# Optimization experiments

Measured on AMD Instinct MI355X. Metric: run time of the kernel, lower is better.

The kernel has to match this reference:

```python
import jax, jax.numpy as jnp
import numpy as np

H = 256  # rnn_size


def setup_inputs() -> dict:
    key = jax.random.key(0)
    ks = jax.random.split(key, 6)
    B, T, F, D = 64, 512, 64, 64
    s_in = 1.0 / np.sqrt(F)
    s_rec = 1.0 / np.sqrt(H)
    return {
        "x": jax.random.normal(ks[0], (B, T, F), jnp.float32),
        "kernel": jax.random.normal(ks[1], (F, 3 * H), jnp.float32) * s_in,
        "recurrent_kernel": jax.random.normal(ks[2], (H, 3 * H), jnp.float32) * s_rec,
        "bias": jax.random.normal(ks[3], (3 * H,), jnp.float32) * 0.01,
        "dense_w": jax.random.normal(ks[4], (H, D), jnp.float32) * s_rec,
        "dense_b": jax.random.normal(ks[5], (D,), jnp.float32) * 0.01,
    }


def _gru_scan(x, kernel, recurrent_kernel, bias):
    B, T, _ = x.shape
    # Pre-project all timesteps: [B, T, 3H]
    xproj = jnp.einsum("btf,fg->btg", x, kernel) + bias
    xproj_t = jnp.transpose(xproj, (1, 0, 2))  # [T, B, 3H]

    def step(h, xt):
        # Keras GRU, reset_after=False: r gates the recurrent matmul of the candidate
        rec = h @ recurrent_kernel  # [B, 3H]
        xz, xr, xh = xt[:, :H], xt[:, H:2 * H], xt[:, 2 * H:]
        rz, rr, rh = rec[:, :H], rec[:, H:2 * H], rec[:, 2 * H:]
        z = jax.nn.sigmoid(xz + rz)
        r = jax.nn.sigmoid(xr + rr)
        hh = jnp.tanh(xh + r * rh)
        h_new = z * h + (1.0 - z) * hh
        return h_new, h_new

    h0 = jnp.zeros((B, H), x.dtype)
    h_last, outs = jax.lax.scan(step, h0, xproj_t)
    return jnp.transpose(outs, (1, 0, 2)), h_last  # [B,T,H], [B,H]


def reference(x, kernel, recurrent_kernel, bias, dense_w, dense_b):
    outputs, h_last = _gru_scan(x, kernel, recurrent_kernel, bias)
    state = jnp.tanh(h_last @ dense_w + dense_b)  # [B, dense_size]
    return outputs, state
```

## Files before the change

kernel.cpp:

```cpp
#include <hip/hip_runtime.h>


typedef _Float16 half2_t __attribute__((ext_vector_type(2)));
typedef _Float16 f16x4_t __attribute__((ext_vector_type(4)));

#define LOG2E 1.4426950408889634f

__device__ __forceinline__ float fast_sigmoid(float x) {
  float e = __builtin_amdgcn_exp2f(-x * LOG2E);
  return __builtin_amdgcn_rcpf(1.0f + e);
}
__device__ __forceinline__ float fast_tanh(float x) {
  float e = __builtin_amdgcn_exp2f(x * (2.0f * LOG2E));
  return 1.0f - 2.0f * __builtin_amdgcn_rcpf(1.0f + e);
}

__global__ __launch_bounds__(256, 4) void xproj_gemm(
    const float* __restrict__ x, const float* __restrict__ kmat,
    const float* __restrict__ bias, _Float16* __restrict__ xp) {
  __shared__ half2_t As2[32][132];
  __shared__ half2_t Bs2[32][132];
  const int tid = threadIdx.x;
  const int rb = blockIdx.x * 128;
  const int cb = blockIdx.y * 128;

  {
    const int k4 = (tid & 15) * 4;
    const int r0 = tid >> 4;
#pragma unroll
    for (int p = 0; p < 8; ++p) {
      int r = r0 + p * 16;
      float4 v = *(const float4*)(x + (size_t)(rb + r) * 64 + k4);
      half2_t lo, hi;
      lo[0] = (_Float16)v.x; lo[1] = (_Float16)v.y;
      hi[0] = (_Float16)v.z; hi[1] = (_Float16)v.w;
      As2[k4 / 2][r] = lo;
      As2[k4 / 2 + 1][r] = hi;
    }
  }
  {
    const int c4 = (tid & 31) * 4;
    const int kp0 = tid >> 5;
#pragma unroll
    for (int p = 0; p < 4; ++p) {
      int kp = kp0 + p * 8;
      float4 va = *(const float4*)(kmat + (size_t)(2 * kp) * 768 + cb + c4);
      float4 vb = *(const float4*)(kmat + (size_t)(2 * kp + 1) * 768 + cb + c4);
      half2_t o0, o1, o2, o3;
      o0[0] = (_Float16)va.x; o0[1] = (_Float16)vb.x;
      o1[0] = (_Float16)va.y; o1[1] = (_Float16)vb.y;
      o2[0] = (_Float16)va.z; o2[1] = (_Float16)vb.z;
      o3[0] = (_Float16)va.w; o3[1] = (_Float16)vb.w;
      Bs2[kp][c4 + 0] = o0;
      Bs2[kp][c4 + 1] = o1;
      Bs2[kp][c4 + 2] = o2;
      Bs2[kp][c4 + 3] = o3;
    }
  }
  __syncthreads();

  const int tx = tid & 15, ty = tid >> 4;
  const int r0 = ty * 8;
  const int c0 = tx * 4;
  float acc[8][8];
  {
    float4 b0 = *(const float4*)(bias + cb + c0);
    float4 b1 = *(const float4*)(bias + cb + 64 + c0);
    float bz[8] = {b0.x, b0.y, b0.z, b0.w, b1.x, b1.y, b1.z, b1.w};
#pragma unroll
    for (int i = 0; i < 8; ++i)
#pragma unroll
      for (int j = 0; j < 8; ++j) acc[i][j] = bz[j];
  }

#pragma unroll 2
  for (int kp = 0; kp < 32; ++kp) {
    half2_t a2[8], b2[8];
    *(int4*)(&a2[0]) = *(const int4*)(&As2[kp][r0]);
    *(int4*)(&a2[4]) = *(const int4*)(&As2[kp][r0 + 4]);
    *(int2*)(&b2[0]) = *(const int2*)(&Bs2[kp][c0]);
    *(int2*)(&b2[2]) = *(const int2*)(&Bs2[kp][c0 + 2]);
    *(int2*)(&b2[4]) = *(const int2*)(&Bs2[kp][64 + c0]);
    *(int2*)(&b2[6]) = *(const int2*)(&Bs2[kp][64 + c0 + 2]);
#pragma unroll
    for (int i = 0; i < 8; ++i)
#pragma unroll
      for (int j = 0; j < 8; ++j)
        acc[i][j] = __builtin_amdgcn_fdot2(a2[i], b2[j], acc[i][j], false);
  }

#pragma unroll
  for (int i = 0; i < 8; ++i) {
    f16x4_t o0, o1;
#pragma unroll
    for (int j = 0; j < 4; ++j) {
      o0[j] = (_Float16)acc[i][j];
      o1[j] = (_Float16)acc[i][4 + j];
    }
    _Float16* dst = xp + (size_t)(rb + r0 + i) * 768 + cb;
    *(f16x4_t*)(dst + c0) = o0;
    *(f16x4_t*)(dst + 64 + c0) = o1;
  }
}

__global__ __launch_bounds__(1024, 4) void gru_scan(
    const _Float16* __restrict__ xp, const float* __restrict__ wr,
    const float* __restrict__ dw, const float* __restrict__ db,
    float* __restrict__ out, float* __restrict__ state) {
  __shared__ float2 part2[768 * 3];
  __shared__ float hbuf[256];
  __shared__ alignas(16) _Float16 hhalf[256];

  const int tid = threadIdx.x;
  const int b = blockIdx.x;
  const int c = tid >> 8;
  const int col = tid & 255;

  half2_t w2[3][32];
#pragma unroll
  for (int q = 0; q < 3; ++q) {
    const float* wp = wr + (size_t)(c * 64) * 768 + col + q * 256;
#pragma unroll
    for (int j = 0; j < 32; ++j) {
      float wa = wp[(size_t)(2 * j) * 768];
      float wb = wp[(size_t)(2 * j + 1) * 768];
      half2_t p;
      p[0] = (_Float16)wa;
      p[1] = (_Float16)wb;
      w2[q][j] = p;
    }
  }
#pragma unroll
  for (int q = 0; q < 3; ++q)
#pragma unroll
    for (int j = 0; j < 32; ++j) asm volatile("" : "+v"(w2[q][j]));

  if (tid < 256) hhalf[tid] = (_Float16)0.0f;
  __syncthreads();

  const _Float16* xpb = xp + (size_t)b * 512 * 768;
  float* outb = out + (size_t)b * 512 * 256;
  const int4* hp2 = (const int4*)hhalf + c * 8;
  float* pw = (float*)part2;
  float hprev = 0.0f;

#pragma unroll 1
  for (int t = 0; t < 512; ++t) {
    _Float16 x0 = (_Float16)0.0f, x1 = (_Float16)0.0f, x2 = (_Float16)0.0f;
    if (tid < 256) {
      if (t) outb[(size_t)(t - 1) * 256 + tid] = hprev;
      const _Float16* xr = xpb + (size_t)t * 768 + tid;
      x0 = xr[0];
      x1 = xr[256];
      x2 = xr[512];
    }

    float a0 = 0.0f, a1 = 0.0f, a2 = 0.0f;
#pragma unroll
    for (int g = 0; g < 8; ++g) {
      int4 hv = hp2[g];
      half2_t p0 = __builtin_bit_cast(half2_t, hv.x);
      half2_t p1 = __builtin_bit_cast(half2_t, hv.y);
      half2_t p2 = __builtin_bit_cast(half2_t, hv.z);
      half2_t p3 = __builtin_bit_cast(half2_t, hv.w);
      a0 = __builtin_amdgcn_fdot2(p0, w2[0][g * 4 + 0], a0, false);
      a0 = __builtin_amdgcn_fdot2(p1, w2[0][g * 4 + 1], a0, false);
      a0 = __builtin_amdgcn_fdot2(p2, w2[0][g * 4 + 2], a0, false);
      a0 = __builtin_amdgcn_fdot2(p3, w2[0][g * 4 + 3], a0, false);
      a1 = __builtin_amdgcn_fdot2(p0, w2[1][g * 4 + 0], a1, false);
      a1 = __builtin_amdgcn_fdot2(p1, w2[1][g * 4 + 1], a1, false);
      a1 = __builtin_amdgcn_fdot2(p2, w2[1][g * 4 + 2], a1, false);
      a1 = __builtin_amdgcn_fdot2(p3, w2[1][g * 4 + 3], a1, false);
      a2 = __builtin_amdgcn_fdot2(p0, w2[2][g * 4 + 0], a2, false);
      a2 = __builtin_amdgcn_fdot2(p1, w2[2][g * 4 + 1], a2, false);
      a2 = __builtin_amdgcn_fdot2(p2, w2[2][g * 4 + 2], a2, false);
      a2 = __builtin_amdgcn_fdot2(p3, w2[2][g * 4 + 3], a2, false);
    }
    pw[col * 6 + c] = a0;
    pw[1536 + col * 6 + c] = a1;
    pw[3072 + col * 6 + c] = a2;
    __syncthreads();

    if (tid < 256) {
      const int i = tid;
      float2 z0 = part2[i * 3 + 0];
      float2 z1 = part2[i * 3 + 1];
      float2 r0 = part2[768 + i * 3 + 0];
      float2 r1 = part2[768 + i * 3 + 1];
      float2 h0 = part2[1536 + i * 3 + 0];
      float2 h1 = part2[1536 + i * 3 + 1];
      float rz = (z0.x + z0.y) + (z1.x + z1.y);
      float rr = (r0.x + r0.y) + (r1.x + r1.y);
      float rh = (h0.x + h0.y) + (h1.x + h1.y);
      float z = fast_sigmoid((float)x0 + rz);
      float r = fast_sigmoid((float)x1 + rr);
      float hh = fast_tanh((float)x2 + r * rh);
      float hnew = z * hprev + (1.0f - z) * hh;
      hprev = hnew;
      hhalf[i] = (_Float16)hnew;
    }
    __syncthreads();
  }

  if (tid < 256) {
    outb[(size_t)511 * 256 + tid] = hprev;
    hbuf[tid] = hprev;
  }
  __syncthreads();

  if (tid < 64) {
    float acc = db[tid];
#pragma unroll 8
    for (int k = 0; k < 256; ++k) acc = fmaf(hbuf[k], dw[k * 64 + tid], acc);
    state[(size_t)b * 64 + tid] = fast_tanh(acc);
  }
}

extern "C" void kernel_launch(void* const* d_in, const int* in_sizes, int n_in,
                              void* d_out, int out_size, void* d_ws,
                              size_t ws_size, hipStream_t stream) {
  const float* x = (const float*)d_in[0];
  const float* kmat = (const float*)d_in[1];
  const float* wr = (const float*)d_in[2];
  const float* bias = (const float*)d_in[3];
  const float* dw = (const float*)d_in[4];
  const float* db = (const float*)d_in[5];

  float* out = (float*)d_out;
  float* state = out + (size_t)64 * 512 * 256;
  _Float16* xp = (_Float16*)d_ws;

  dim3 gg(32768 / 128, 768 / 128);
  xproj_gemm<<<gg, 256, 0, stream>>>(x, kmat, bias, xp);
  gru_scan<<<64, 1024, 0, stream>>>(xp, wr, dw, db, out, state);
}
```

Measured before the change: 660.9 us.

## Process four batch rows per block in GRU scan, reusing register weights

Each scan block now handles four batch sequences, reusing the per-thread fp16 recurrent weights held in registers across all four. Each thread computes partial matvecs for all four batches and then runs the gate update for its own batch element, so all 1024 threads do elementwise work. The grid shrinks from 64 to 16 blocks, which quadruples the serial per-step dot-product work and enlarges shared memory. The empty asm statements that kept the weights pinned in registers are also removed.

New measurement: 2.055 ms. 211% more time.

```diff
diff --git a/kernel.cpp b/kernel.cpp
--- a/kernel.cpp
+++ b/kernel.cpp
@@ -107,19 +107,19 @@
     const _Float16* __restrict__ xp, const float* __restrict__ wr,
     const float* __restrict__ dw, const float* __restrict__ db,
     float* __restrict__ out, float* __restrict__ state) {
-  __shared__ float2 part2[768 * 3];
-  __shared__ float hbuf[256];
-  __shared__ alignas(16) _Float16 hhalf[256];
+  __shared__ float pw[4 * 768 * 6];
+  __shared__ alignas(16) _Float16 hhalf[4][256];
+  __shared__ float hbuf[4][256];
 
   const int tid = threadIdx.x;
-  const int b = blockIdx.x;
-  const int c = tid >> 8;
+  const int bg = blockIdx.x;
+  const int kc = tid >> 8;
   const int col = tid & 255;
 
   half2_t w2[3][32];
 #pragma unroll
   for (int q = 0; q < 3; ++q) {
-    const float* wp = wr + (size_t)(c * 64) * 768 + col + q * 256;
+    const float* wp = wr + (size_t)(kc * 64) * 768 + col + q * 256;
 #pragma unroll
     for (int j = 0; j < 32; ++j) {
       float wa = wp[(size_t)(2 * j) * 768];
@@ -130,65 +130,64 @@
       w2[q][j] = p;
     }
   }
-#pragma unroll
-  for (int q = 0; q < 3; ++q)
-#pragma unroll
-    for (int j = 0; j < 32; ++j) asm volatile("" : "+v"(w2[q][j]));
-
-  if (tid < 256) hhalf[tid] = (_Float16)0.0f;
+
+  hhalf[kc][col] = (_Float16)0.0f;
   __syncthreads();
 
-  const _Float16* xpb = xp + (size_t)b * 512 * 768;
-  float* outb = out + (size_t)b * 512 * 256;
-  const int4* hp2 = (const int4*)hhalf + c * 8;
-  float* pw = (float*)part2;
+  const _Float16* xpb = xp + (size_t)(bg * 4 + kc) * 512 * 768;
+  float* outb = out + (size_t)(bg * 4 + kc) * 512 * 256;
   float hprev = 0.0f;
 
 #pragma unroll 1
   for (int t = 0; t < 512; ++t) {
-    _Float16 x0 = (_Float16)0.0f, x1 = (_Float16)0.0f, x2 = (_Float16)0.0f;
-    if (tid < 256) {
-      if (t) outb[(size_t)(t - 1) * 256 + tid] = hprev;
-      const _Float16* xr = xpb + (size_t)t * 768 + tid;
-      x0 = xr[0];
-      x1 = xr[256];
-      x2 = xr[512];
-    }
-
-    float a0 = 0.0f, a1 = 0.0f, a2 = 0.0f;
-#pragma unroll
-    for (int g = 0; g < 8; ++g) {
-      int4 hv = hp2[g];
-      half2_t p0 = __builtin_bit_cast(half2_t, hv.x);
-      half2_t p1 = __builtin_bit_cast(half2_t, hv.y);
-      half2_t p2 = __builtin_bit_cast(half2_t, hv.z);
-      half2_t p3 = __builtin_bit_cast(half2_t, hv.w);
-      a0 = __builtin_amdgcn_fdot2(p0, w2[0][g * 4 + 0], a0, false);
-      a0 = __builtin_amdgcn_fdot2(p1, w2[0][g * 4 + 1], a0, false);
-      a0 = __builtin_amdgcn_fdot2(p2, w2[0][g * 4 + 2], a0, false);
-      a0 = __builtin_amdgcn_fdot2(p3, w2[0][g * 4 + 3], a0, false);
-      a1 = __builtin_amdgcn_fdot2(p0, w2[1][g * 4 + 0], a1, false);
-      a1 = __builtin_amdgcn_fdot2(p1, w2[1][g * 4 + 1], a1, false);
-      a1 = __builtin_amdgcn_fdot2(p2, w2[1][g * 4 + 2], a1, false);
-      a1 = __builtin_amdgcn_fdot2(p3, w2[1][g * 4 + 3], a1, false);
-      a2 = __builtin_amdgcn_fdot2(p0, w2[2][g * 4 + 0], a2, false);
-      a2 = __builtin_amdgcn_fdot2(p1, w2[2][g * 4 + 1], a2, false);
-      a2 = __builtin_amdgcn_fdot2(p2, w2[2][g * 4 + 2], a2, false);
-      a2 = __builtin_amdgcn_fdot2(p3, w2[2][g * 4 + 3], a2, false);
-    }
-    pw[col * 6 + c] = a0;
-    pw[1536 + col * 6 + c] = a1;
-    pw[3072 + col * 6 + c] = a2;
+    _Float16 x0, x1, x2;
+    {
+      if (t) outb[(size_t)(t - 1) * 256 + col] = hprev;
+      const _Float16* xq = xpb + (size_t)t * 768 + col;
+      x0 = xq[0];
+      x1 = xq[256];
+      x2 = xq[512];
+    }
+
+#pragma unroll
+    for (int b = 0; b < 4; ++b) {
+      const int4* hp = (const int4*)&hhalf[b][0] + kc * 8;
+      float a0 = 0.0f, a1 = 0.0f, a2 = 0.0f;
+#pragma unroll
+      for (int g = 0; g < 8; ++g) {
+        int4 hv = hp[g];
+        half2_t p0 = __builtin_bit_cast(half2_t, hv.x);
+        half2_t p1 = __builtin_bit_cast(half2_t, hv.y);
+        half2_t p2 = __builtin_bit_cast(half2_t, hv.z);
+        half2_t p3 = __builtin_bit_cast(half2_t, hv.w);
+        a0 = __builtin_amdgcn_fdot2(p0, w2[0][g * 4 + 0], a0, false);
+        a0 = __builtin_amdgcn_fdot2(p1, w2[0][g * 4 + 1], a0, false);
+        a0 = __builtin_amdgcn_fdot2(p2, w2[0][g * 4 + 2], a0, false);
+        a0 = __builtin_amdgcn_fdot2(p3, w2[0][g * 4 + 3], a0, false);
+        a1 = __builtin_amdgcn_fdot2(p0, w2[1][g * 4 + 0], a1, false);
+        a1 = __builtin_amdgcn_fdot2(p1, w2[1][g * 4 + 1], a1, false);
+        a1 = __builtin_amdgcn_fdot2(p2, w2[1][g * 4 + 2], a1, false);
+        a1 = __builtin_amdgcn_fdot2(p3, w2[1][g * 4 + 3], a1, false);
+        a2 = __builtin_amdgcn_fdot2(p0, w2[2][g * 4 + 0], a2, false);
+        a2 = __builtin_amdgcn_fdot2(p1, w2[2][g * 4 + 1], a2, false);
+        a2 = __builtin_amdgcn_fdot2(p2, w2[2][g * 4 + 2], a2, false);
+        a2 = __builtin_amdgcn_fdot2(p3, w2[2][g * 4 + 3], a2, false);
+      }
+      float* pb = pw + b * 4608;
+      pb[(size_t)col * 6 + kc] = a0;
+      pb[(size_t)(256 + col) * 6 + kc] = a1;
+      pb[(size_t)(512 + col) * 6 + kc] = a2;
+    }
     __syncthreads();
 
-    if (tid < 256) {
-      const int i = tid;
-      float2 z0 = part2[i * 3 + 0];
-      float2 z1 = part2[i * 3 + 1];
-      float2 r0 = part2[768 + i * 3 + 0];
-      float2 r1 = part2[768 + i * 3 + 1];
-      float2 h0 = part2[1536 + i * 3 + 0];
-      float2 h1 = part2[1536 + i * 3 + 1];
+    {
+      const float2* pb = (const float2*)(pw + kc * 4608);
+      float2 z0 = pb[col * 3 + 0];
+      float2 z1 = pb[col * 3 + 1];
+      float2 r0 = pb[(256 + col) * 3 + 0];
+      float2 r1 = pb[(256 + col) * 3 + 1];
+      float2 h0 = pb[(512 + col) * 3 + 0];
+      float2 h1 = pb[(512 + col) * 3 + 1];
       float rz = (z0.x + z0.y) + (z1.x + z1.y);
       float rr = (r0.x + r0.y) + (r1.x + r1.y);
       float rh = (h0.x + h0.y) + (h1.x + h1.y);
@@ -197,22 +196,23 @@
       float hh = fast_tanh((float)x2 + r * rh);
       float hnew = z * hprev + (1.0f - z) * hh;
       hprev = hnew;
-      hhalf[i] = (_Float16)hnew;
+      hhalf[kc][col] = (_Float16)hnew;
     }
     __syncthreads();
   }
 
+  outb[(size_t)511 * 256 + col] = hprev;
+  hbuf[kc][col] = hprev;
+  __syncthreads();
+
   if (tid < 256) {
-    outb[(size_t)511 * 256 + tid] = hprev;
-    hbuf[tid] = hprev;
-  }
-  __syncthreads();
-
-  if (tid < 64) {
-    float acc = db[tid];
+    const int bt = tid >> 6;
+    const int d = tid & 63;
+    float acc = db[d];
 #pragma unroll 8
-    for (int k = 0; k < 256; ++k) acc = fmaf(hbuf[k], dw[k * 64 + tid], acc);
-    state[(size_t)b * 64 + tid] = fast_tanh(acc);
+    for (int k = 0; k < 256; ++k)
+      acc = fmaf(hbuf[bt][k], dw[k * 64 + d], acc);
+    state[(size_t)(bg * 4 + bt) * 64 + d] = fast_tanh(acc);
   }
 }
 
@@ -232,5 +232,5 @@
 
   dim3 gg(32768 / 128, 768 / 128);
   xproj_gemm<<<gg, 256, 0, stream>>>(x, kmat, bias, xp);
-  gru_scan<<<64, 1024, 0, stream>>>(xp, wr, dw, db, out, state);
-}
+  gru_scan<<<16, 1024, 0, stream>>>(xp, wr, dw, db, out, state);
+}
```

## Rewrite input projection GEMM with MFMA 16x16x32 f16 instructions

Applied to the files above, without the earlier changes.

Replaces the LDS-tiled fdot2 input projection GEMM with a register-only MFMA version. Each wave loads A and B fragments straight from global memory, converts them to fp16 and runs mfma_f32_16x16x32_f16, then adds the bias and stores fp16. This drops the shared-memory staging and the __syncthreads, and the output stores now become strided 2-byte writes. The serial gru_scan kernel most likely dominates total time, so the overall effect is limited.

New measurement: 654.5 us. About the same (-1.0%).

```diff
diff --git a/kernel.cpp b/kernel.cpp
--- a/kernel.cpp
+++ b/kernel.cpp
@@ -3,6 +3,8 @@
 
 typedef _Float16 half2_t __attribute__((ext_vector_type(2)));
 typedef _Float16 f16x4_t __attribute__((ext_vector_type(4)));
+typedef _Float16 f16x8_t __attribute__((ext_vector_type(8)));
+typedef float f32x4_t __attribute__((ext_vector_type(4)));
 
 #define LOG2E 1.4426950408889634f
 
@@ -15,92 +17,67 @@
   return 1.0f - 2.0f * __builtin_amdgcn_rcpf(1.0f + e);
 }
 
-__global__ __launch_bounds__(256, 4) void xproj_gemm(
+__global__ __launch_bounds__(256) void xproj_gemm(
     const float* __restrict__ x, const float* __restrict__ kmat,
     const float* __restrict__ bias, _Float16* __restrict__ xp) {
-  __shared__ half2_t As2[32][132];
-  __shared__ half2_t Bs2[32][132];
   const int tid = threadIdx.x;
+  const int lane = tid & 63;
+  const int w = tid >> 6;
+  const int q = lane >> 4;
+  const int r15 = lane & 15;
   const int rb = blockIdx.x * 128;
   const int cb = blockIdx.y * 128;
 
-  {
-    const int k4 = (tid & 15) * 4;
-    const int r0 = tid >> 4;
-#pragma unroll
-    for (int p = 0; p < 8; ++p) {
-      int r = r0 + p * 16;
-      float4 v = *(const float4*)(x + (size_t)(rb + r) * 64 + k4);
-      half2_t lo, hi;
-      lo[0] = (_Float16)v.x; lo[1] = (_Float16)v.y;
-      hi[0] = (_Float16)v.z; hi[1] = (_Float16)v.w;
-      As2[k4 / 2][r] = lo;
-      As2[k4 / 2 + 1][r] = hi;
-    }
-  }
-  {
-    const int c4 = (tid & 31) * 4;
-    const int kp0 = tid >> 5;
-#pragma unroll
-    for (int p = 0; p < 4; ++p) {
-      int kp = kp0 + p * 8;
-      float4 va = *(const float4*)(kmat + (size_t)(2 * kp) * 768 + cb + c4);
-      float4 vb = *(const float4*)(kmat + (size_t)(2 * kp + 1) * 768 + cb + c4);
-      half2_t o0, o1, o2, o3;
-      o0[0] = (_Float16)va.x; o0[1] = (_Float16)vb.x;
-      o1[0] = (_Float16)va.y; o1[1] = (_Float16)vb.y;
-      o2[0] = (_Float16)va.z; o2[1] = (_Float16)vb.z;
-      o3[0] = (_Float16)va.w; o3[1] = (_Float16)vb.w;
-      Bs2[kp][c4 + 0] = o0;
-      Bs2[kp][c4 + 1] = o1;
-      Bs2[kp][c4 + 2] = o2;
-      Bs2[kp][c4 + 3] = o3;
-    }
-  }
-  __syncthreads();
-
-  const int tx = tid & 15, ty = tid >> 4;
-  const int r0 = ty * 8;
-  const int c0 = tx * 4;
-  float acc[8][8];
-  {
-    float4 b0 = *(const float4*)(bias + cb + c0);
-    float4 b1 = *(const float4*)(bias + cb + 64 + c0);
-    float bz[8] = {b0.x, b0.y, b0.z, b0.w, b1.x, b1.y, b1.z, b1.w};
-#pragma unroll
-    for (int i = 0; i < 8; ++i)
-#pragma unroll
-      for (int j = 0; j < 8; ++j) acc[i][j] = bz[j];
-  }
-
-#pragma unroll 2
-  for (int kp = 0; kp < 32; ++kp) {
-    half2_t a2[8], b2[8];
-    *(int4*)(&a2[0]) = *(const int4*)(&As2[kp][r0]);
-    *(int4*)(&a2[4]) = *(const int4*)(&As2[kp][r0 + 4]);
-    *(int2*)(&b2[0]) = *(const int2*)(&Bs2[kp][c0]);
-    *(int2*)(&b2[2]) = *(const int2*)(&Bs2[kp][c0 + 2]);
-    *(int2*)(&b2[4]) = *(const int2*)(&Bs2[kp][64 + c0]);
-    *(int2*)(&b2[6]) = *(const int2*)(&Bs2[kp][64 + c0 + 2]);
-#pragma unroll
-    for (int i = 0; i < 8; ++i)
-#pragma unroll
-      for (int j = 0; j < 8; ++j)
-        acc[i][j] = __builtin_amdgcn_fdot2(a2[i], b2[j], acc[i][j], false);
-  }
-
-#pragma unroll
-  for (int i = 0; i < 8; ++i) {
-    f16x4_t o0, o1;
-#pragma unroll
-    for (int j = 0; j < 4; ++j) {
-      o0[j] = (_Float16)acc[i][j];
-      o1[j] = (_Float16)acc[i][4 + j];
-    }
-    _Float16* dst = xp + (size_t)(rb + r0 + i) * 768 + cb;
-    *(f16x4_t*)(dst + c0) = o0;
-    *(f16x4_t*)(dst + 64 + c0) = o1;
-  }
+  f16x8_t bf[8][2];
+#pragma unroll
+  for (int nt = 0; nt < 8; ++nt)
+#pragma unroll
+    for (int kt = 0; kt < 2; ++kt) {
+      const float* bp =
+          kmat + (size_t)(kt * 32 + q * 8) * 768 + cb + nt * 16 + r15;
+      f16x8_t v;
+#pragma unroll
+      for (int j = 0; j < 8; ++j) v[j] = (_Float16)bp[(size_t)j * 768];
+      bf[nt][kt] = v;
+    }
+
+  f16x8_t af[2][2];
+#pragma unroll
+  for (int mt = 0; mt < 2; ++mt)
+#pragma unroll
+    for (int kt = 0; kt < 2; ++kt) {
+      const float* ap =
+          x + (size_t)(rb + w * 32 + mt * 16 + r15) * 64 + kt * 32 + q * 8;
+      float4 v0 = *(const float4*)(ap);
+      float4 v1 = *(const float4*)(ap + 4);
+      f16x8_t v;
+      v[0] = (_Float16)v0.x; v[1] = (_Float16)v0.y;
+      v[2] = (_Float16)v0.z; v[3] = (_Float16)v0.w;
+      v[4] = (_Float16)v1.x; v[5] = (_Float16)v1.y;
+      v[6] = (_Float16)v1.z; v[7] = (_Float16)v1.w;
+      af[mt][kt] = v;
+    }
+
+  float bz[8];
+#pragma unroll
+  for (int nt = 0; nt < 8; ++nt) bz[nt] = bias[cb + nt * 16 + r15];
+
+#pragma unroll
+  for (int mt = 0; mt < 2; ++mt)
+#pragma unroll
+    for (int nt = 0; nt < 8; ++nt) {
+      f32x4_t acc = {0.f, 0.f, 0.f, 0.f};
+      acc = __builtin_amdgcn_mfma_f32_16x16x32_f16(af[mt][0], bf[nt][0], acc,
+                                                   0, 0, 0);
+      acc = __builtin_amdgcn_mfma_f32_16x16x32_f16(af[mt][1], bf[nt][1], acc,
+                                                   0, 0, 0);
+      _Float16* dp =
+          xp + (size_t)(rb + w * 32 + mt * 16 + q * 4) * 768 + cb + nt * 16 +
+          r15;
+#pragma unroll
+      for (int r = 0; r < 4; ++r)
+        dp[(size_t)r * 768] = (_Float16)(acc[r] + bz[nt]);
+    }
 }
 
 __global__ __launch_bounds__(1024, 4) void gru_scan(
```
